# Optimization experiments

Hardware: AMD Instinct MI355X
Metric: run time of the kernel (lower is better)

## Reference

```python
import jax, jax.numpy as jnp
import numpy as np

N_PARTS = 24


def setup_inputs() -> dict:
    key = jax.random.key(0)
    k1, k2, k3, k4 = jax.random.split(key, 4)
    B, C, R = 8, 16, 512
    H = W = 512
    tex = jax.random.normal(k1, (B, C, R, R), dtype=jnp.float32)
    # iuv: channel 0 = part id in [0, 24] (0 == background), channels 1,2 = UV bytes in [0, 255]
    part = jax.random.randint(k2, (B, 1, H, W), 0, N_PARTS + 1, dtype=jnp.int32)
    uv = jax.random.randint(k3, (B, 2, H, W), 0, 256, dtype=jnp.int32)
    iuv = jnp.concatenate([part, uv], axis=1)
    lut = jax.random.uniform(k4, (N_PARTS, 256, 256, 2), dtype=jnp.float32)
    return {"tex": tex, "iuv": iuv, "lut": lut, "tex_res": R}


def reference(tex, iuv, lut, tex_res):
    # tex: [B, C, R, R], iuv: [B, 3, H, W] int, lut: [24, 256, 256, 2]
    B = tex.shape[0]
    mask = iuv[:, 0] > 0                                   # [B, H, W]
    i = jnp.clip(iuv[:, 0] - 1, 0, lut.shape[0] - 1)       # part index, clamped for masked-out pixels
    u = jnp.clip(iuv[:, 1].astype(jnp.float32) / 255.0, 0.0, 1.0)
    v = jnp.clip(iuv[:, 2].astype(jnp.float32) / 255.0, 0.0, 1.0)
    ui = jnp.round(u * 255.0).astype(jnp.int32)
    vi = jnp.round(v * 255.0).astype(jnp.int32)
    uv_smpl = lut[i, vi, ui]                               # [B, H, W, 2]
    u_I = jnp.round(uv_smpl[..., 0] * (tex_res - 1)).astype(jnp.int32)
    v_I = jnp.round((1.0 - uv_smpl[..., 1]) * (tex_res - 1)).astype(jnp.int32)
    b_idx = jnp.arange(B)[:, None, None]                   # [B, 1, 1]
    gathered = tex[b_idx, :, v_I, u_I]                     # [B, H, W, C]
    out = jnp.where(mask[..., None], gathered, jnp.zeros((), tex.dtype))
    return jnp.transpose(out, (0, 3, 1, 2))                # [B, C, H, W]
```

## Files before the change

### kernel.cpp

```cpp
#include <hip/hip_runtime.h>


#define N_PARTS 24

__global__ __launch_bounds__(256) void dp_offsets_kernel(
    const int*   __restrict__ iuv,
    const float* __restrict__ lut,
    int*         __restrict__ offs,
    int R)
{
    constexpr int H = 512, W = 512;
    const float scale = (float)(R - 1);

    const int t = blockIdx.x * blockDim.x + threadIdx.x;
    const size_t hw = (size_t)H * W;
    const int pix4 = t * 4;
    const int b = pix4 >> 18;
    const int p = pix4 & (int)(hw - 1);

    const size_t ibase = (size_t)b * 3 * hw + p;
    const int4 p4 = *(const int4*)(iuv + ibase);
    const int4 u4 = *(const int4*)(iuv + ibase + hw);
    const int4 v4 = *(const int4*)(iuv + ibase + 2 * hw);

    const int parts[4] = {p4.x, p4.y, p4.z, p4.w};
    const int us[4]    = {u4.x, u4.y, u4.z, u4.w};
    const int vs[4]    = {v4.x, v4.y, v4.z, v4.w};

    int4 o4;
    int* o = &o4.x;
    #pragma unroll
    for (int j = 0; j < 4; ++j) {
        int i = parts[j] - 1;
        i = i < 0 ? 0 : (i > N_PARTS - 1 ? N_PARTS - 1 : i);
        const float fu = fminf(fmaxf((float)us[j] / 255.0f, 0.0f), 1.0f);
        const float fv = fminf(fmaxf((float)vs[j] / 255.0f, 0.0f), 1.0f);
        const int ui = (int)rintf(fu * 255.0f);
        const int vi = (int)rintf(fv * 255.0f);
        const float2 s = *(const float2*)(lut + (((size_t)i * 256 + vi) * 256 + ui) * 2);
        const int uI = (int)rintf(s.x * scale);
        const int vI = (int)rintf((1.0f - s.y) * scale);
        o[j] = (parts[j] > 0) ? (vI * R + uI) : -1;
    }
    *(int4*)(offs + (size_t)b * hw + p) = o4;
}

__global__ __launch_bounds__(256) void dp_gather_kernel(
    const float* __restrict__ tex,
    const int*   __restrict__ offs,
    float*       __restrict__ out,
    int R)
{
    constexpr int C = 16, H = 512, W = 512;
    const size_t hw    = (size_t)H * W;
    const size_t plane = (size_t)R * R;

    const int bid  = blockIdx.x;
    const int xcd  = bid & 7;
    const int slot = bid >> 3;
    const int pl_local = slot >> 8;
    const int inner    = slot & 255;
    const int pidx = xcd * 16 + pl_local;
    const int b = pidx >> 4;
    const int c = pidx & 15;

    const int px = inner * 1024 + threadIdx.x * 4;

    const int4 o4 = *(const int4*)(offs + (size_t)b * hw + px);
    const float* tc = tex + ((size_t)b * C + c) * plane;

    float4 r;
    r.x = (o4.x >= 0) ? tc[o4.x] : 0.0f;
    r.y = (o4.y >= 0) ? tc[o4.y] : 0.0f;
    r.z = (o4.z >= 0) ? tc[o4.z] : 0.0f;
    r.w = (o4.w >= 0) ? tc[o4.w] : 0.0f;

    *(float4*)(out + ((size_t)b * C + c) * hw + px) = r;
}

__global__ __launch_bounds__(256) void dp_fused_kernel(
    const float* __restrict__ tex,
    const int*   __restrict__ iuv,
    const float* __restrict__ lut,
    float*       __restrict__ out,
    int R)
{
    constexpr int B = 8, C = 16, H = 512, W = 512;
    const float scale = (float)(R - 1);
    const int t  = blockIdx.x * blockDim.x + threadIdx.x;
    const int WP = W / 4;
    const int w4  = (t % WP) * 4;
    const int tmp = t / WP;
    const int h   = tmp % H;
    const int b   = tmp / H;
    if (b >= B) return;

    const size_t hw    = (size_t)H * W;
    const size_t ibase = (size_t)b * 3 * hw + (size_t)h * W + w4;
    const int4 p4 = *(const int4*)(iuv + ibase);
    const int4 u4 = *(const int4*)(iuv + ibase + hw);
    const int4 v4 = *(const int4*)(iuv + ibase + 2 * hw);

    const int parts[4] = {p4.x, p4.y, p4.z, p4.w};
    const int us[4]    = {u4.x, u4.y, u4.z, u4.w};
    const int vs[4]    = {v4.x, v4.y, v4.z, v4.w};

    int  off[4]; bool m[4];
    #pragma unroll
    for (int j = 0; j < 4; ++j) {
        m[j] = parts[j] > 0;
        int i = parts[j] - 1;
        i = i < 0 ? 0 : (i > N_PARTS - 1 ? N_PARTS - 1 : i);
        const float fu = fminf(fmaxf((float)us[j] / 255.0f, 0.0f), 1.0f);
        const float fv = fminf(fmaxf((float)vs[j] / 255.0f, 0.0f), 1.0f);
        const int ui = (int)rintf(fu * 255.0f);
        const int vi = (int)rintf(fv * 255.0f);
        const float2 s = *(const float2*)(lut + (((size_t)i * 256 + vi) * 256 + ui) * 2);
        off[j] = ((int)rintf((1.0f - s.y) * scale)) * R + (int)rintf(s.x * scale);
    }

    const size_t plane = (size_t)R * R;
    const float* texb  = tex + (size_t)b * C * plane;
    float*       outb  = out + ((size_t)b * C * H + h) * W + w4;

    #pragma unroll
    for (int c = 0; c < C; ++c) {
        const float* tc = texb + (size_t)c * plane;
        float4 o;
        o.x = m[0] ? tc[off[0]] : 0.0f;
        o.y = m[1] ? tc[off[1]] : 0.0f;
        o.z = m[2] ? tc[off[2]] : 0.0f;
        o.w = m[3] ? tc[off[3]] : 0.0f;
        *(float4*)(outb + (size_t)c * hw) = o;
    }
}

extern "C" void kernel_launch(void* const* d_in, const int* in_sizes, int n_in,
                              void* d_out, int out_size, void* d_ws, size_t ws_size,
                              hipStream_t stream) {
    const float* tex = (const float*)d_in[0];
    const int*   iuv = (const int*)d_in[1];
    const float* lut = (const float*)d_in[2];
    float*       out = (float*)d_out;

    constexpr int B = 8, C = 16, H = 512, W = 512;
    int R = 512;
    {
        long long pe = (long long)in_sizes[0] / (B * C);
        int r = 1; while ((long long)(r + 1) * (r + 1) <= pe) ++r;
        R = r;
    }

    const size_t offs_bytes = (size_t)B * H * W * sizeof(int);
    if (ws_size >= offs_bytes) {
        int* offs = (int*)d_ws;
        dp_offsets_kernel<<<dim3((B * H * W / 4 + 255) / 256), dim3(256), 0, stream>>>(
            iuv, lut, offs, R);
        dp_gather_kernel<<<dim3(B * C * (H * W / 1024)), dim3(256), 0, stream>>>(
            tex, offs, out, R);
    } else {
        const int threads = B * H * (W / 4);
        dp_fused_kernel<<<dim3((threads + 255) / 256), dim3(256), 0, stream>>>(
            tex, iuv, lut, out, R);
    }
}
```

Baseline: 403.1 us.

## Transpose texture to channel-last and gather 64-byte texels per pixel

Adds a prep kernel that transposes the texture from [B,C,R,R] to [B,R,R,C] in workspace, sharing its launch with the offset computation by interleaving block roles. A new gather kernel then loads all 16 channels for a pixel as four contiguous float4 reads and transposes them through LDS into coalesced channel-planar output. This replaces 16 scattered 4-byte reads per pixel with one 64-byte contiguous read. The cost is a full 128 MB read and write of the texture per call, and the fused fallback path is removed.

```diff
diff --git a/kernel.cpp b/kernel.cpp
--- a/kernel.cpp
+++ b/kernel.cpp
@@ -2,6 +2,138 @@
 
 
 #define N_PARTS 24
+
+__global__ __launch_bounds__(256) void dp_prep_kernel(
+    const float* __restrict__ tex,
+    const int*   __restrict__ iuv,
+    const float* __restrict__ lut,
+    float*       __restrict__ texT,
+    int*         __restrict__ offs)
+{
+    constexpr int C = 16, H = 512, W = 512, R = 512;
+    constexpr size_t hw    = (size_t)H * W;
+    constexpr size_t plane = (size_t)R * R;
+    __shared__ float lds[16 * 516];
+
+    const int bid = blockIdx.x;
+    const int g   = bid / 3;
+    const int r3  = bid - g * 3;
+
+    if (r3 != 2) {
+        const int tid = g * 2 + r3;
+        const int b  = tid >> 9;
+        const int ty = tid & 511;
+        const float* src = tex + (size_t)b * C * plane + (size_t)ty * R;
+        const int t = threadIdx.x;
+
+        #pragma unroll
+        for (int k = 0; k < 8; ++k) {
+            const int f  = k * 256 + t;
+            const int c  = f >> 7;
+            const int x4 = f & 127;
+            const float4 v = *(const float4*)(src + (size_t)c * plane + x4 * 4);
+            *(float4*)&lds[c * 516 + x4 * 4] = v;
+        }
+        __syncthreads();
+        float* dst = texT + ((size_t)b * plane + (size_t)ty * R) * C;
+        #pragma unroll
+        for (int k = 0; k < 8; ++k) {
+            const int f  = k * 256 + t;
+            const int x  = f >> 2;
+            const int c0 = (f & 3) * 4;
+            float4 v;
+            v.x = lds[(c0 + 0) * 516 + x];
+            v.y = lds[(c0 + 1) * 516 + x];
+            v.z = lds[(c0 + 2) * 516 + x];
+            v.w = lds[(c0 + 3) * 516 + x];
+            *(float4*)(dst + (size_t)f * 4) = v;
+        }
+    } else {
+        const float scale = (float)(R - 1);
+        const int t = g * 256 + threadIdx.x;
+        const int pix4 = t * 4;
+        const int b = pix4 >> 18;
+        const int p = pix4 & (int)(hw - 1);
+
+        const size_t ibase = (size_t)b * 3 * hw + p;
+        const int4 p4 = *(const int4*)(iuv + ibase);
+        const int4 u4 = *(const int4*)(iuv + ibase + hw);
+        const int4 v4 = *(const int4*)(iuv + ibase + 2 * hw);
+
+        const int parts[4] = {p4.x, p4.y, p4.z, p4.w};
+        const int us[4]    = {u4.x, u4.y, u4.z, u4.w};
+        const int vs[4]    = {v4.x, v4.y, v4.z, v4.w};
+
+        int4 o4; int* o = &o4.x;
+        #pragma unroll
+        for (int j = 0; j < 4; ++j) {
+            int i = parts[j] - 1;
+            i = i < 0 ? 0 : (i > N_PARTS - 1 ? N_PARTS - 1 : i);
+            const float fu = fminf(fmaxf((float)us[j] / 255.0f, 0.0f), 1.0f);
+            const float fv = fminf(fmaxf((float)vs[j] / 255.0f, 0.0f), 1.0f);
+            const int ui = (int)rintf(fu * 255.0f);
+            const int vi = (int)rintf(fv * 255.0f);
+            const float2 s = *(const float2*)(lut + (((size_t)i * 256 + vi) * 256 + ui) * 2);
+            const int uI = (int)rintf(s.x * scale);
+            const int vI = (int)rintf((1.0f - s.y) * scale);
+            o[j] = (parts[j] > 0) ? (vI * R + uI) : -1;
+        }
+        *(int4*)(offs + (size_t)b * hw + p) = o4;
+    }
+}
+
+__global__ __launch_bounds__(256) void dp_gatherT_kernel(
+    const float* __restrict__ texT,
+    const int*   __restrict__ offs,
+    float*       __restrict__ out)
+{
+    constexpr int C = 16;
+    constexpr size_t HW = 512 * 512;
+    __shared__ float lds[16 * 256];
+
+    const int b     = blockIdx.x & 7;
+    const int inner = blockIdx.x >> 3;
+    const int base  = inner * 1024;
+
+    const float* tb   = texT + (size_t)b * HW * C;
+    const int*   ob   = offs + (size_t)b * HW + base;
+    float*       outb = out  + (size_t)b * C * HW + base;
+    const int t = threadIdx.x;
+
+    for (int tile = 0; tile < 4; ++tile) {
+        const int p = tile * 256 + t;
+        const int o = ob[p];
+        const bool m = o >= 0;
+        const float4* src = (const float4*)(tb + (size_t)(m ? o : 0) * C);
+        float4 r0 = src[0];
+        float4 r1 = src[1];
+        float4 r2 = src[2];
+        float4 r3 = src[3];
+        if (!m) {
+            r0 = r1 = r2 = r3 = make_float4(0.f, 0.f, 0.f, 0.f);
+        }
+
+        if (tile) __syncthreads();
+        lds[ 0 * 256 + t] = r0.x;  lds[ 1 * 256 + t] = r0.y;
+        lds[ 2 * 256 + t] = r0.z;  lds[ 3 * 256 + t] = r0.w;
+        lds[ 4 * 256 + t] = r1.x;  lds[ 5 * 256 + t] = r1.y;
+        lds[ 6 * 256 + t] = r1.z;  lds[ 7 * 256 + t] = r1.w;
+        lds[ 8 * 256 + t] = r2.x;  lds[ 9 * 256 + t] = r2.y;
+        lds[10 * 256 + t] = r2.z;  lds[11 * 256 + t] = r2.w;
+        lds[12 * 256 + t] = r3.x;  lds[13 * 256 + t] = r3.y;
+        lds[14 * 256 + t] = r3.z;  lds[15 * 256 + t] = r3.w;
+        __syncthreads();
+
+        #pragma unroll
+        for (int k = 0; k < 4; ++k) {
+            const int idx = k * 256 + t;
+            const int c   = idx >> 6;
+            const int p4  = idx & 63;
+            const float4 v = *(const float4*)&lds[c * 256 + p4 * 4];
+            *(float4*)(outb + (size_t)c * HW + tile * 256 + p4 * 4) = v;
+        }
+    }
+}
 
 __global__ __launch_bounds__(256) void dp_offsets_kernel(
     const int*   __restrict__ iuv,
@@ -11,9 +143,8 @@
 {
     constexpr int H = 512, W = 512;
     const float scale = (float)(R - 1);
-
+    const size_t hw = (size_t)H * W;
     const int t = blockIdx.x * blockDim.x + threadIdx.x;
-    const size_t hw = (size_t)H * W;
     const int pix4 = t * 4;
     const int b = pix4 >> 18;
     const int p = pix4 & (int)(hw - 1);
@@ -27,8 +158,7 @@
     const int us[4]    = {u4.x, u4.y, u4.z, u4.w};
     const int vs[4]    = {v4.x, v4.y, v4.z, v4.w};
 
-    int4 o4;
-    int* o = &o4.x;
+    int4 o4; int* o = &o4.x;
     #pragma unroll
     for (int j = 0; j < 4; ++j) {
         int i = parts[j] - 1;
@@ -78,63 +208,6 @@
     *(float4*)(out + ((size_t)b * C + c) * hw + px) = r;
 }
 
-__global__ __launch_bounds__(256) void dp_fused_kernel(
-    const float* __restrict__ tex,
-    const int*   __restrict__ iuv,
-    const float* __restrict__ lut,
-    float*       __restrict__ out,
-    int R)
-{
-    constexpr int B = 8, C = 16, H = 512, W = 512;
-    const float scale = (float)(R - 1);
-    const int t  = blockIdx.x * blockDim.x + threadIdx.x;
-    const int WP = W / 4;
-    const int w4  = (t % WP) * 4;
-    const int tmp = t / WP;
-    const int h   = tmp % H;
-    const int b   = tmp / H;
-    if (b >= B) return;
-
-    const size_t hw    = (size_t)H * W;
-    const size_t ibase = (size_t)b * 3 * hw + (size_t)h * W + w4;
-    const int4 p4 = *(const int4*)(iuv + ibase);
-    const int4 u4 = *(const int4*)(iuv + ibase + hw);
-    const int4 v4 = *(const int4*)(iuv + ibase + 2 * hw);
-
-    const int parts[4] = {p4.x, p4.y, p4.z, p4.w};
-    const int us[4]    = {u4.x, u4.y, u4.z, u4.w};
-    const int vs[4]    = {v4.x, v4.y, v4.z, v4.w};
-
-    int  off[4]; bool m[4];
-    #pragma unroll
-    for (int j = 0; j < 4; ++j) {
-        m[j] = parts[j] > 0;
-        int i = parts[j] - 1;
-        i = i < 0 ? 0 : (i > N_PARTS - 1 ? N_PARTS - 1 : i);
-        const float fu = fminf(fmaxf((float)us[j] / 255.0f, 0.0f), 1.0f);
-        const float fv = fminf(fmaxf((float)vs[j] / 255.0f, 0.0f), 1.0f);
-        const int ui = (int)rintf(fu * 255.0f);
-        const int vi = (int)rintf(fv * 255.0f);
-        const float2 s = *(const float2*)(lut + (((size_t)i * 256 + vi) * 256 + ui) * 2);
-        off[j] = ((int)rintf((1.0f - s.y) * scale)) * R + (int)rintf(s.x * scale);
-    }
-
-    const size_t plane = (size_t)R * R;
-    const float* texb  = tex + (size_t)b * C * plane;
-    float*       outb  = out + ((size_t)b * C * H + h) * W + w4;
-
-    #pragma unroll
-    for (int c = 0; c < C; ++c) {
-        const float* tc = texb + (size_t)c * plane;
-        float4 o;
-        o.x = m[0] ? tc[off[0]] : 0.0f;
-        o.y = m[1] ? tc[off[1]] : 0.0f;
-        o.z = m[2] ? tc[off[2]] : 0.0f;
-        o.w = m[3] ? tc[off[3]] : 0.0f;
-        *(float4*)(outb + (size_t)c * hw) = o;
-    }
-}
-
 extern "C" void kernel_launch(void* const* d_in, const int* in_sizes, int n_in,
                               void* d_out, int out_size, void* d_ws, size_t ws_size,
                               hipStream_t stream) {
@@ -151,16 +224,21 @@
         R = r;
     }
 
+    const size_t texT_bytes = (size_t)B * R * R * C * sizeof(float);
     const size_t offs_bytes = (size_t)B * H * W * sizeof(int);
-    if (ws_size >= offs_bytes) {
+
+    if (R == 512 && ws_size >= texT_bytes + offs_bytes) {
+        float* texT = (float*)d_ws;
+        int*   offs = (int*)((char*)d_ws + texT_bytes);
+        dp_prep_kernel<<<dim3(6144), dim3(256), 0, stream>>>(
+            tex, iuv, lut, texT, offs);
+        dp_gatherT_kernel<<<dim3(2048), dim3(256), 0, stream>>>(
+            texT, offs, out);
+    } else if (ws_size >= offs_bytes) {
         int* offs = (int*)d_ws;
-        dp_offsets_kernel<<<dim3((B * H * W / 4 + 255) / 256), dim3(256), 0, stream>>>(
+        dp_offsets_kernel<<<dim3(B * H * W / 4 / 256), dim3(256), 0, stream>>>(
             iuv, lut, offs, R);
         dp_gather_kernel<<<dim3(B * C * (H * W / 1024)), dim3(256), 0, stream>>>(
             tex, offs, out, R);
-    } else {
-        const int threads = B * H * (W / 4);
-        dp_fused_kernel<<<dim3((threads + 255) / 256), dim3(256), 0, stream>>>(
-            tex, iuv, lut, out, R);
-    }
-}
+    }
+}
```

New measurement: 344.1 us. -14.7%, faster.
